# Kernel optimization log

Measured on AMD Instinct MI355X. Metric: run time of the kernel, lower is better.

The kernel has to match this reference:

```python
import jax, jax.numpy as jnp
import numpy as np

# Segmented tensor-product configuration (matches init_kwargs)
NUM_SEG = 32   # segments per operand
MUL = 128      # multiplicity ('u' axis) of operand0 / output segments
D = 3          # irrep dimension (2l+1 with l=1) for i, j, k axes
NUM_PATHS = 64
BATCH = 2048


def setup_inputs() -> dict:
    key = jax.random.key(0)
    k0, k1, k2, k3, k4, k5 = jax.random.split(key, 6)
    x0 = jax.random.normal(k0, (BATCH, NUM_SEG * MUL * D), dtype=jnp.float32)
    x1 = jax.random.normal(k1, (BATCH, NUM_SEG * D), dtype=jnp.float32)
    coeff = jax.random.normal(k2, (NUM_PATHS, D, D, D), dtype=jnp.float32)
    idx0 = jax.random.randint(k3, (NUM_PATHS,), 0, NUM_SEG, dtype=jnp.int32)
    idx1 = jax.random.randint(k4, (NUM_PATHS,), 0, NUM_SEG, dtype=jnp.int32)
    idx2 = jax.random.randint(k5, (NUM_PATHS,), 0, NUM_SEG, dtype=jnp.int32)
    return {"x0": x0, "x1": x1, "coeff": coeff,
            "idx0": idx0, "idx1": idx1, "idx2": idx2}


def reference(x0, x1, coeff, idx0, idx1, idx2):
    # Segmented CG tensor product:
    #   out[seg2][u,k] += sum_{paths p with idx2[p]==seg2}
    #       sum_ij x0[idx0[p]][u,i] * x1[idx1[p]][j] * coeff[p][i,j,k]
    B = x0.shape[0]
    x0s = x0.reshape(B, NUM_SEG, MUL, D)   # 'ui' segments
    x1s = x1.reshape(B, NUM_SEG, D)        # 'j' segments
    # gather input segments per path
    x0p = x0s[:, idx0]                     # (B, P, MUL, D)
    x1p = x1s[:, idx1]                     # (B, P, D)
    # per-path contraction with path coefficients, path axis first for scatter
    contrib = jnp.einsum('bpui,bpj,pijk->pbuk', x0p, x1p, coeff)
    # scatter-add contributions into output segments
    out_seg = jax.ops.segment_sum(contrib, idx2, num_segments=NUM_SEG)  # (S, B, MUL, D)
    out = jnp.transpose(out_seg, (1, 0, 2, 3)).reshape(B, NUM_SEG * MUL * D)
    return out
```

## Files before the change

### kernel.cpp

```cpp
#include <hip/hip_runtime.h>

#define NUM_SEG 32
#define MUL 128
#define D 3
#define NUM_PATHS 64
#define ROW (NUM_SEG * MUL * D)
#define SEGF (MUL * D)
#define SEG_HF 192
#define PE_STRIDE 64
#define M_PAD 12

typedef float v2f __attribute__((ext_vector_type(2)));
typedef float v4f __attribute__((ext_vector_type(4)));

__global__ __launch_bounds__(64) void ftp_setup(
    const float* __restrict__ x1, const float* __restrict__ coeff,
    const int* __restrict__ idx0, const int* __restrict__ idx1,
    const int* __restrict__ idx2,
    unsigned int* __restrict__ sched, float* __restrict__ m)
{
    const int tid = threadIdx.x;
    if (blockIdx.x == 0) {
        __shared__ int lcnt[NUM_SEG];
        __shared__ unsigned int lpe[NUM_SEG][PE_STRIDE];
        if (tid < NUM_SEG) lcnt[tid] = 0;
        __syncthreads();
        {
            const int p   = tid;
            const int s2  = idx2[p];
            const int pos = atomicAdd(&lcnt[s2], 1);
            lpe[s2][pos]  = (unsigned int)(idx0[p] | (p << 8));
        }
        __syncthreads();
        if (tid < NUM_SEG) sched[tid] = (unsigned int)lcnt[tid];
        for (int j = tid; j < NUM_SEG * PE_STRIDE; j += 64) {
            const int s = j / PE_STRIDE, t = j % PE_STRIDE;
            sched[NUM_SEG + j] = (t < lcnt[s]) ? lpe[s][t] : 0u;
        }
    } else {
        const int b = blockIdx.x - 1;
        const int p = tid;
        const float* xr = x1 + (size_t)b * (NUM_SEG * D) + idx1[p] * D;
        const float j0 = xr[0], j1 = xr[1], j2 = xr[2];
        const float* cf = coeff + p * 27;
        float mv[M_PAD];
        #pragma unroll
        for (int i = 0; i < D; ++i)
            #pragma unroll
            for (int k = 0; k < D; ++k)
                mv[i * 3 + k] = j0 * cf[i * 9 + k]
                              + j1 * cf[i * 9 + 3 + k]
                              + j2 * cf[i * 9 + 6 + k];
        mv[9] = 0.f; mv[10] = 0.f; mv[11] = 0.f;
        float* mp = m + ((size_t)b * NUM_PATHS + p) * M_PAD;
        *(v4f*)(mp)     = *(const v4f*)(mv);
        *(v4f*)(mp + 4) = *(const v4f*)(mv + 4);
        *(v4f*)(mp + 8) = *(const v4f*)(mv + 8);
    }
}

__global__ __launch_bounds__(256) void ftp_main(
    const float* __restrict__ x0, const unsigned int* __restrict__ sched,
    const float* __restrict__ m, float* __restrict__ out)
{
    const int bid = blockIdx.x;
    const int b   = bid >> 1;
    const int h   = bid & 1;
    const int tid = threadIdx.x;
    const int qq  = tid & 15;
    const int ss  = tid >> 4;

    const float* __restrict__ xb = x0  + (size_t)b * ROW + h * SEG_HF + qq * 12;
    float* __restrict__       ob = out + (size_t)b * ROW + h * SEG_HF + qq * 12;
    const float* __restrict__ mb = m + (size_t)b * NUM_PATHS * M_PAD;
    const unsigned int* __restrict__ pe = sched + NUM_SEG;

    const int n0 = (int)sched[ss];
    const int n1 = (int)sched[ss + 16];

    #pragma unroll
    for (int si = 0; si < 2; ++si) {
        const int s = ss + si * 16;
        const int n = si ? n1 : n0;
        const unsigned int* __restrict__ pes = pe + s * PE_STRIDE;
        float a00 = 0, a01 = 0, a02 = 0, a10 = 0, a11 = 0, a12 = 0;
        float a20 = 0, a21 = 0, a22 = 0, a30 = 0, a31 = 0, a32 = 0;
        for (int t = 0; t < n; ++t) {
            const unsigned e = pes[t];
            const float* xs = xb + (e & 255u) * SEGF;
            const v4f X0 = *(const v4f*)(xs);
            const v4f X1 = *(const v4f*)(xs + 4);
            const v4f X2 = *(const v4f*)(xs + 8);
            const float* mp = mb + (e >> 8) * M_PAD;
            const v4f MA = *(const v4f*)(mp);
            const v4f MB = *(const v4f*)(mp + 4);
            const float m22 = mp[8];
            a00 += X0.x * MA.x + X0.y * MA.w + X0.z * MB.z;
            a01 += X0.x * MA.y + X0.y * MB.x + X0.z * MB.w;
            a02 += X0.x * MA.z + X0.y * MB.y + X0.z * m22;
            a10 += X0.w * MA.x + X1.x * MA.w + X1.y * MB.z;
            a11 += X0.w * MA.y + X1.x * MB.x + X1.y * MB.w;
            a12 += X0.w * MA.z + X1.x * MB.y + X1.y * m22;
            a20 += X1.z * MA.x + X1.w * MA.w + X2.x * MB.z;
            a21 += X1.z * MA.y + X1.w * MB.x + X2.x * MB.w;
            a22 += X1.z * MA.z + X1.w * MB.y + X2.x * m22;
            a30 += X2.y * MA.x + X2.z * MA.w + X2.w * MB.z;
            a31 += X2.y * MA.y + X2.z * MB.x + X2.w * MB.w;
            a32 += X2.y * MA.z + X2.z * MB.y + X2.w * m22;
        }
        float* o = ob + s * SEGF;
        v4f O0 = {a00, a01, a02, a10};
        v4f O1 = {a11, a12, a20, a21};
        v4f O2 = {a22, a30, a31, a32};
        *(v4f*)(o)     = O0;
        *(v4f*)(o + 4) = O1;
        *(v4f*)(o + 8) = O2;
    }
}

#define HALF_F4 1536

__global__ __launch_bounds__(256) void ftp_kernel(
    const float* __restrict__ x0, const float* __restrict__ x1,
    const float* __restrict__ coeff, const int* __restrict__ idx0,
    const int* __restrict__ idx1, const int* __restrict__ idx2,
    float* __restrict__ out)
{
    const int bid = blockIdx.x;
    const int b   = bid >> 1;
    const int h   = bid & 1;
    const int tid = threadIdx.x;

    __shared__ v4f   s_x0[HALF_F4];
    __shared__ float s_m[NUM_PATHS][9];
    __shared__ unsigned short s_pe[NUM_SEG][NUM_PATHS];
    __shared__ int   s_cnt[NUM_SEG];

    if (tid < NUM_SEG) s_cnt[tid] = 0;
    __syncthreads();

    const v4f* __restrict__ src = (const v4f*)(x0 + (size_t)b * ROW);
    #pragma unroll
    for (int j = 0; j < 6; ++j) {
        const int f     = j * 256 + tid;
        const int seg   = f / 48;
        const int inner = f - seg * 48;
        s_x0[f] = src[seg * 96 + h * 48 + inner];
    }

    if (tid < NUM_PATHS) {
        const int p  = tid;
        const int s0 = idx0[p];
        const int i1 = idx1[p];
        const int s2 = idx2[p];
        const int pos = atomicAdd(&s_cnt[s2], 1);
        s_pe[s2][pos] = (unsigned short)(s0 | (p << 8));

        const float* xr = x1 + (size_t)b * (NUM_SEG * D) + i1 * D;
        const float j0 = xr[0], j1 = xr[1], j2 = xr[2];
        const float* cf = coeff + p * 27;
        #pragma unroll
        for (int i = 0; i < D; ++i)
            #pragma unroll
            for (int k = 0; k < D; ++k)
                s_m[p][i * 3 + k] = j0 * cf[i * 9 + k]
                                  + j1 * cf[i * 9 + 3 + k]
                                  + j2 * cf[i * 9 + 6 + k];
    }
    __syncthreads();

    const int q  = tid & 31;
    const int ss = tid >> 5;
    float* __restrict__ ob = out + (size_t)b * ROW + h * SEG_HF + q * 6;
    const float* __restrict__ sx = (const float*)s_x0;

    #pragma unroll
    for (int si = 0; si < 4; ++si) {
        const int s = ss + si * 8;
        float a00 = 0, a01 = 0, a02 = 0, a10 = 0, a11 = 0, a12 = 0;
        const int n = s_cnt[s];
        for (int t = 0; t < n; ++t) {
            const int e = s_pe[s][t];
            const float* xs = sx + (e & 255) * SEG_HF + q * 6;
            const float u00 = xs[0], u01 = xs[1], u02 = xs[2];
            const float u10 = xs[3], u11 = xs[4], u12 = xs[5];
            const float* mm = s_m[e >> 8];
            a00 += u00 * mm[0] + u01 * mm[3] + u02 * mm[6];
            a01 += u00 * mm[1] + u01 * mm[4] + u02 * mm[7];
            a02 += u00 * mm[2] + u01 * mm[5] + u02 * mm[8];
            a10 += u10 * mm[0] + u11 * mm[3] + u12 * mm[6];
            a11 += u10 * mm[1] + u11 * mm[4] + u12 * mm[7];
            a12 += u10 * mm[2] + u11 * mm[5] + u12 * mm[8];
        }
        float* o = ob + s * SEGF;
        v2f O0 = {a00, a01}, O1 = {a02, a10}, O2 = {a11, a12};
        *(v2f*)(o + 0) = O0;
        *(v2f*)(o + 2) = O1;
        *(v2f*)(o + 4) = O2;
    }
}

extern "C" void kernel_launch(void* const* d_in, const int* in_sizes, int n_in,
                              void* d_out, int out_size, void* d_ws, size_t ws_size,
                              hipStream_t stream) {
    const float* x0    = (const float*)d_in[0];
    const float* x1    = (const float*)d_in[1];
    const float* coeff = (const float*)d_in[2];
    const int*   idx0  = (const int*)d_in[3];
    const int*   idx1  = (const int*)d_in[4];
    const int*   idx2  = (const int*)d_in[5];
    float* out = (float*)d_out;

    const int B = in_sizes[0] / ROW;

    const size_t schedBytes = (size_t)(NUM_SEG + NUM_SEG * PE_STRIDE) * sizeof(unsigned int);
    const size_t schedPad   = (schedBytes + 255) & ~(size_t)255;
    const size_t mBytes     = (size_t)B * NUM_PATHS * M_PAD * sizeof(float);

    if (ws_size >= schedPad + mBytes) {
        unsigned int* sched = (unsigned int*)d_ws;
        float*        m     = (float*)((char*)d_ws + schedPad);
        ftp_setup<<<B + 1, 64, 0, stream>>>(x1, coeff, idx0, idx1, idx2, sched, m);
        ftp_main<<<B * 2, 256, 0, stream>>>(x0, sched, m, out);
    } else {
        ftp_kernel<<<B * 2, 256, 0, stream>>>(x0, x1, coeff, idx0, idx1, idx2, out);
    }
}
```

Measured before the change: 214.9 us.

## Stage x0 and path matrices in LDS with compact, count-sorted schedule

The main kernel now copies each batch-half of x0 into LDS with global_load_lds and loads the precomputed per-path 3x3 matrices and a compact CSR-style schedule into shared memory, instead of reading x0 and m directly from global memory per path. The setup kernel builds the schedule as offsets plus a packed entry list, sorts segments by path count so heavily loaded segments are spread across waves, and stores m unpadded at 9 floats per path. This aims to replace repeated gathered global loads with LDS reads and to balance work. The cost is a larger LDS footprint that may limit occupancy, plus an extra barrier.

```diff
diff --git a/kernel.cpp b/kernel.cpp
--- a/kernel.cpp
+++ b/kernel.cpp
@@ -7,8 +7,6 @@
 #define ROW (NUM_SEG * MUL * D)
 #define SEGF (MUL * D)
 #define SEG_HF 192
-#define PE_STRIDE 64
-#define M_PAD 12
 
 typedef float v2f __attribute__((ext_vector_type(2)));
 typedef float v4f __attribute__((ext_vector_type(4)));
@@ -22,20 +20,38 @@
     const int tid = threadIdx.x;
     if (blockIdx.x == 0) {
         __shared__ int lcnt[NUM_SEG];
-        __shared__ unsigned int lpe[NUM_SEG][PE_STRIDE];
+        __shared__ int loff[NUM_SEG];
+        __shared__ int lperm[NUM_SEG];
+        __shared__ unsigned short lent[NUM_PATHS];
         if (tid < NUM_SEG) lcnt[tid] = 0;
         __syncthreads();
-        {
-            const int p   = tid;
-            const int s2  = idx2[p];
-            const int pos = atomicAdd(&lcnt[s2], 1);
-            lpe[s2][pos]  = (unsigned int)(idx0[p] | (p << 8));
-        }
-        __syncthreads();
-        if (tid < NUM_SEG) sched[tid] = (unsigned int)lcnt[tid];
-        for (int j = tid; j < NUM_SEG * PE_STRIDE; j += 64) {
-            const int s = j / PE_STRIDE, t = j % PE_STRIDE;
-            sched[NUM_SEG + j] = (t < lcnt[s]) ? lpe[s][t] : 0u;
+        const int p   = tid;
+        const int s2  = idx2[p];
+        const int pos = atomicAdd(&lcnt[s2], 1);
+        __syncthreads();
+        if (tid == 0) {
+            int off = 0;
+            for (int s = 0; s < NUM_SEG; ++s) { loff[s] = off; off += lcnt[s]; }
+            int perm[NUM_SEG];
+            for (int s = 0; s < NUM_SEG; ++s) perm[s] = s;
+            for (int i = 1; i < NUM_SEG; ++i) {
+                int v = perm[i], cv = lcnt[v], j = i - 1;
+                while (j >= 0 && lcnt[perm[j]] < cv) { perm[j + 1] = perm[j]; --j; }
+                perm[j + 1] = v;
+            }
+            for (int s = 0; s < NUM_SEG; ++s) lperm[s] = perm[s];
+        }
+        __syncthreads();
+        lent[loff[s2] + pos] = (unsigned short)(idx0[p] | (p << 8));
+        __syncthreads();
+        if (tid < NUM_SEG) {
+            const int sg = lperm[tid];
+            sched[tid] = (unsigned)lcnt[sg] | ((unsigned)loff[sg] << 8)
+                       | ((unsigned)sg << 16);
+        }
+        if (tid < NUM_PATHS / 2) {
+            sched[NUM_SEG + tid] = (unsigned)lent[2 * tid]
+                                 | ((unsigned)lent[2 * tid + 1] << 16);
         }
     } else {
         const int b = blockIdx.x - 1;
@@ -43,23 +59,18 @@
         const float* xr = x1 + (size_t)b * (NUM_SEG * D) + idx1[p] * D;
         const float j0 = xr[0], j1 = xr[1], j2 = xr[2];
         const float* cf = coeff + p * 27;
-        float mv[M_PAD];
+        float* mp = m + (size_t)b * (NUM_PATHS * 9) + p * 9;
         #pragma unroll
         for (int i = 0; i < D; ++i)
             #pragma unroll
             for (int k = 0; k < D; ++k)
-                mv[i * 3 + k] = j0 * cf[i * 9 + k]
+                mp[i * 3 + k] = j0 * cf[i * 9 + k]
                               + j1 * cf[i * 9 + 3 + k]
                               + j2 * cf[i * 9 + 6 + k];
-        mv[9] = 0.f; mv[10] = 0.f; mv[11] = 0.f;
-        float* mp = m + ((size_t)b * NUM_PATHS + p) * M_PAD;
-        *(v4f*)(mp)     = *(const v4f*)(mv);
-        *(v4f*)(mp + 4) = *(const v4f*)(mv + 4);
-        *(v4f*)(mp + 8) = *(const v4f*)(mv + 8);
-    }
-}
-
-__global__ __launch_bounds__(256) void ftp_main(
+    }
+}
+
+__global__ __launch_bounds__(256, 6) void ftp_main(
     const float* __restrict__ x0, const unsigned int* __restrict__ sched,
     const float* __restrict__ m, float* __restrict__ out)
 {
@@ -67,54 +78,65 @@
     const int b   = bid >> 1;
     const int h   = bid & 1;
     const int tid = threadIdx.x;
-    const int qq  = tid & 15;
-    const int ss  = tid >> 4;
-
-    const float* __restrict__ xb = x0  + (size_t)b * ROW + h * SEG_HF + qq * 12;
-    float* __restrict__       ob = out + (size_t)b * ROW + h * SEG_HF + qq * 12;
-    const float* __restrict__ mb = m + (size_t)b * NUM_PATHS * M_PAD;
-    const unsigned int* __restrict__ pe = sched + NUM_SEG;
-
-    const int n0 = (int)sched[ss];
-    const int n1 = (int)sched[ss + 16];
-
-    #pragma unroll
-    for (int si = 0; si < 2; ++si) {
-        const int s = ss + si * 16;
-        const int n = si ? n1 : n0;
-        const unsigned int* __restrict__ pes = pe + s * PE_STRIDE;
+
+    __shared__ float s_x0[NUM_SEG * SEG_HF];
+    __shared__ float s_m[NUM_PATHS][9];
+    __shared__ unsigned int s_sched[NUM_SEG];
+    __shared__ unsigned int s_entw[NUM_PATHS / 2];
+
+    const v4f* __restrict__ srcb = (const v4f*)(x0 + (size_t)b * ROW);
+    #pragma unroll
+    for (int j = 0; j < 6; ++j) {
+        const int F   = j * 256 + tid;
+        const int seg = F / 48;
+        const int in4 = F - seg * 48;
+        const v4f* gp = srcb + seg * 96 + h * 48 + in4;
+        __builtin_amdgcn_global_load_lds(
+            (const __attribute__((address_space(1))) void*)gp,
+            (__attribute__((address_space(3))) void*)((v4f*)s_x0 + F),
+            16, 0, 0);
+    }
+
+    if (tid < 144) {
+        const v4f* mg = (const v4f*)(m + (size_t)b * (NUM_PATHS * 9));
+        ((v4f*)s_m)[tid] = mg[tid];
+    } else if (tid < 176) {
+        s_sched[tid - 144] = sched[tid - 144];
+    } else if (tid < 208) {
+        s_entw[tid - 176] = sched[NUM_SEG + (tid - 176)];
+    }
+    __syncthreads();
+
+    const int q  = tid & 31;
+    const int ss = tid >> 5;
+    const unsigned short* s_ent = (const unsigned short*)s_entw;
+    float* __restrict__ ob = out + (size_t)b * ROW + h * SEG_HF + q * 6;
+
+    #pragma unroll
+    for (int si = 0; si < 4; ++si) {
+        const unsigned sc = s_sched[ss + si * 8];
+        const int n   = sc & 255;
+        const int off = (sc >> 8) & 255;
+        const int s   = sc >> 16;
         float a00 = 0, a01 = 0, a02 = 0, a10 = 0, a11 = 0, a12 = 0;
-        float a20 = 0, a21 = 0, a22 = 0, a30 = 0, a31 = 0, a32 = 0;
         for (int t = 0; t < n; ++t) {
-            const unsigned e = pes[t];
-            const float* xs = xb + (e & 255u) * SEGF;
-            const v4f X0 = *(const v4f*)(xs);
-            const v4f X1 = *(const v4f*)(xs + 4);
-            const v4f X2 = *(const v4f*)(xs + 8);
-            const float* mp = mb + (e >> 8) * M_PAD;
-            const v4f MA = *(const v4f*)(mp);
-            const v4f MB = *(const v4f*)(mp + 4);
-            const float m22 = mp[8];
-            a00 += X0.x * MA.x + X0.y * MA.w + X0.z * MB.z;
-            a01 += X0.x * MA.y + X0.y * MB.x + X0.z * MB.w;
-            a02 += X0.x * MA.z + X0.y * MB.y + X0.z * m22;
-            a10 += X0.w * MA.x + X1.x * MA.w + X1.y * MB.z;
-            a11 += X0.w * MA.y + X1.x * MB.x + X1.y * MB.w;
-            a12 += X0.w * MA.z + X1.x * MB.y + X1.y * m22;
-            a20 += X1.z * MA.x + X1.w * MA.w + X2.x * MB.z;
-            a21 += X1.z * MA.y + X1.w * MB.x + X2.x * MB.w;
-            a22 += X1.z * MA.z + X1.w * MB.y + X2.x * m22;
-            a30 += X2.y * MA.x + X2.z * MA.w + X2.w * MB.z;
-            a31 += X2.y * MA.y + X2.z * MB.x + X2.w * MB.w;
-            a32 += X2.y * MA.z + X2.z * MB.y + X2.w * m22;
+            const int e = s_ent[off + t];
+            const float* xs = s_x0 + (e & 255) * SEG_HF + q * 6;
+            const float u00 = xs[0], u01 = xs[1], u02 = xs[2];
+            const float u10 = xs[3], u11 = xs[4], u12 = xs[5];
+            const float* mm = s_m[e >> 8];
+            a00 += u00 * mm[0] + u01 * mm[3] + u02 * mm[6];
+            a01 += u00 * mm[1] + u01 * mm[4] + u02 * mm[7];
+            a02 += u00 * mm[2] + u01 * mm[5] + u02 * mm[8];
+            a10 += u10 * mm[0] + u11 * mm[3] + u12 * mm[6];
+            a11 += u10 * mm[1] + u11 * mm[4] + u12 * mm[7];
+            a12 += u10 * mm[2] + u11 * mm[5] + u12 * mm[8];
         }
         float* o = ob + s * SEGF;
-        v4f O0 = {a00, a01, a02, a10};
-        v4f O1 = {a11, a12, a20, a21};
-        v4f O2 = {a22, a30, a31, a32};
-        *(v4f*)(o)     = O0;
-        *(v4f*)(o + 4) = O1;
-        *(v4f*)(o + 8) = O2;
+        v2f O0 = {a00, a01}, O1 = {a02, a10}, O2 = {a11, a12};
+        *(v2f*)(o + 0) = O0;
+        *(v2f*)(o + 2) = O1;
+        *(v2f*)(o + 4) = O2;
     }
 }
 
@@ -213,9 +235,9 @@
 
     const int B = in_sizes[0] / ROW;
 
-    const size_t schedBytes = (size_t)(NUM_SEG + NUM_SEG * PE_STRIDE) * sizeof(unsigned int);
+    const size_t schedBytes = (size_t)(NUM_SEG + NUM_PATHS / 2) * sizeof(unsigned int);
     const size_t schedPad   = (schedBytes + 255) & ~(size_t)255;
-    const size_t mBytes     = (size_t)B * NUM_PATHS * M_PAD * sizeof(float);
+    const size_t mBytes     = (size_t)B * NUM_PATHS * 9 * sizeof(float);
 
     if (ws_size >= schedPad + mBytes) {
         unsigned int* sched = (unsigned int*)d_ws;
```

New measurement: 216.0 us. About the same (+0.5%).
